# Performance work log

Hardware: AMD Instinct MI355X
Metric: run time of the kernel (lower is better)

## Reference

```python
import jax, jax.numpy as jnp
import numpy as np

B, N, E, ED, H, HID, OUT = 128, 100, 3200, 8, 4, 16, 32


def _ln(x, g, b):
    m = x.mean(-1, keepdims=True)
    v = ((x - m) ** 2).mean(-1, keepdims=True)
    return (x - m) / jnp.sqrt(v + 1e-5) * g + b


def _seg_softmax(logits, seg, n):
    # logits: [Etot, H], seg: [Etot] target node ids
    m = jax.ops.segment_max(logits, seg, num_segments=n)
    ex = jnp.exp(logits - m[seg])
    s = jax.ops.segment_sum(ex, seg, num_segments=n)
    return ex / (s[seg] + 1e-16)


def _tconv(x, src, dst, ea, Wq, bq, Wk, bk, Wv, bv, We, Ws, bs, heads, ch, n):
    # PyG TransformerConv, concat=False, root_weight=True, beta=False
    q = (x @ Wq.T + bq).reshape(-1, heads, ch)
    k = (x @ Wk.T + bk).reshape(-1, heads, ch)
    v = (x @ Wv.T + bv).reshape(-1, heads, ch)
    e = (ea @ We.T).reshape(-1, heads, ch)
    alpha = (q[dst] * (k[src] + e)).sum(-1) / jnp.sqrt(jnp.float32(ch))  # [Etot,H]
    alpha = _seg_softmax(alpha, dst, n)
    msg = (v[src] + e) * alpha[..., None]
    out = jax.ops.segment_sum(msg, dst, num_segments=n)  # [n,H,ch]
    out = out.mean(axis=1)  # concat=False -> head mean
    return out + x @ Ws.T + bs


def setup_inputs() -> dict:
    key = jax.random.key(0)
    ks = jax.random.split(key, 32)
    d = {}
    d['nodes_feats'] = jax.random.randint(ks[0], (B, N, 1), 0, 5).astype(jnp.float32)
    d['edge_index'] = jax.random.randint(ks[1], (B, 2, E), 0, N).astype(jnp.int32)
    d['edge_attr'] = jax.random.normal(ks[2], (B, E, ED), jnp.float32)
    d['agent_id'] = jax.random.randint(ks[3], (B, 1), 0, N).astype(jnp.int32)
    s = 0.1
    d['entity_embed'] = jax.random.normal(ks[4], (5, 4), jnp.float32)
    d['W1'] = jax.random.normal(ks[5], (HID, 4 + ED), jnp.float32) * s
    d['b1'] = jnp.zeros((HID,), jnp.float32)
    d['W2'] = jax.random.normal(ks[6], (HID, HID), jnp.float32) * s
    d['b2'] = jnp.zeros((HID,), jnp.float32)
    d['W3'] = jax.random.normal(ks[7], (HID, HID), jnp.float32) * s
    d['b3'] = jnp.zeros((HID,), jnp.float32)
    d['ln_g'] = jnp.ones((HID,), jnp.float32)
    d['ln_b'] = jnp.zeros((HID,), jnp.float32)
    i = 8
    for pre, ch, outd in (('g1', HID, HID), ('g2', OUT, OUT)):
        d[pre + '_Wq'] = jax.random.normal(ks[i + 0], (H * ch, HID), jnp.float32) * s
        d[pre + '_bq'] = jnp.zeros((H * ch,), jnp.float32)
        d[pre + '_Wk'] = jax.random.normal(ks[i + 1], (H * ch, HID), jnp.float32) * s
        d[pre + '_bk'] = jnp.zeros((H * ch,), jnp.float32)
        d[pre + '_Wv'] = jax.random.normal(ks[i + 2], (H * ch, HID), jnp.float32) * s
        d[pre + '_bv'] = jnp.zeros((H * ch,), jnp.float32)
        d[pre + '_We'] = jax.random.normal(ks[i + 3], (H * ch, ED), jnp.float32) * s
        d[pre + '_Ws'] = jax.random.normal(ks[i + 4], (outd, HID), jnp.float32) * s
        d[pre + '_bs'] = jnp.zeros((outd,), jnp.float32)
        i += 5
    return d


def reference(nodes_feats, edge_index, edge_attr, agent_id, entity_embed,
              W1, b1, W2, b2, W3, b3, ln_g, ln_b,
              g1_Wq, g1_bq, g1_Wk, g1_bk, g1_Wv, g1_bv, g1_We, g1_Ws, g1_bs,
              g2_Wq, g2_bq, g2_Wk, g2_bk, g2_Wv, g2_bv, g2_We, g2_Ws, g2_bs):
    n_tot = B * N
    # batched graph -> flat graph with per-batch node offsets
    offs = (jnp.arange(B, dtype=edge_index.dtype) * N)[:, None, None]
    ei = (edge_index + offs).transpose(1, 0, 2).reshape(2, -1)  # [2, B*E]
    src, dst = ei[0], ei[1]
    x = nodes_feats.reshape(-1, 1)            # [n_tot, 1]
    ea = edge_attr.reshape(-1, ED)            # [B*E, ED]

    # Embedding message-passing layer (aggr='add')
    etype = x[:, 0].astype(jnp.int32)[src]
    emb = entity_embed[etype]                  # [Etot, 4]
    h = jnp.concatenate([emb, ea], axis=1)
    h = _ln(jax.nn.relu(h @ W1.T + b1), ln_g, ln_b)
    h = _ln(jax.nn.relu(h @ W2.T + b2), ln_g, ln_b)
    h = _ln(jax.nn.relu(h @ W3.T + b3), ln_g, ln_b)
    z = jax.ops.segment_sum(h, dst, num_segments=n_tot)  # [n_tot, 16]

    a = _tconv(z, src, dst, ea, g1_Wq, g1_bq, g1_Wk, g1_bk, g1_Wv, g1_bv,
               g1_We, g1_Ws, g1_bs, H, HID, n_tot)
    a = _tconv(a, src, dst, ea, g2_Wq, g2_bq, g2_Wk, g2_bk, g2_Wv, g2_bv,
               g2_We, g2_Ws, g2_bs, H, OUT, n_tot)
    a = jax.nn.relu(a).reshape(B, N, OUT)
    # graph_aggr == 'agent': gather the agent node per batch
    out = jnp.take_along_axis(a, agent_id[:, :, None].astype(jnp.int32), axis=1)
    return out[:, 0, :]  # [B, OUT]
```

## Files before the change

kernel.cpp:

```cpp
#include <hip/hip_runtime.h>
#include <math.h>
#include <stdint.h>

#define Bb   128
#define Nn   100
#define Ee   3200
#define NTOT (Bb*Nn)
#define ETOT (Bb*Ee)



__global__ __launch_bounds__(1024) void k_csr(const int* __restrict__ ei,
                                              const int* __restrict__ agent,
                                              int* __restrict__ off,
                                              int2* __restrict__ cpair,
                                              int* __restrict__ mark)
{
    int b = ((blockIdx.x & 7) << 4) + (blockIdx.x >> 3);
    int t = threadIdx.x;
    __shared__ int s_src[Ee];
    __shared__ int s_dst[Ee];
    __shared__ int cnt[128];
    __shared__ int exc[128];
    __shared__ int cur[128];
    if (t < 128) cnt[t] = 0;
    if (t < Nn) mark[b * Nn + t] = 0;
    __syncthreads();
    const int* eis = ei + (size_t)b * 2 * Ee;
    const int* eid = eis + Ee;
    for (int e = t; e < Ee; e += 1024) {
        int s = eis[e];
        int d = eid[e];
        s_src[e] = s;
        s_dst[e] = d;
        atomicAdd(&cnt[d], 1);
    }
    __syncthreads();
    if (t < 64) {
        int c0 = cnt[2 * t];
        int c1 = cnt[2 * t + 1];
        int p = c0 + c1;
#pragma unroll
        for (int d = 1; d < 64; d <<= 1) {
            int v = __shfl_up(p, d);
            if (t >= d) p += v;
        }
        exc[2 * t]     = p - c0 - c1;
        exc[2 * t + 1] = p - c1;
        cur[2 * t]     = p - c0 - c1;
        cur[2 * t + 1] = p - c1;
    }
    __syncthreads();
    if (t < Nn) off[b * Nn + t] = b * Ee + exc[t];
    if (b == Bb - 1 && t == 0) off[NTOT] = ETOT;
    for (int e = t; e < Ee; e += 1024) {
        int d = s_dst[e];
        int idx = atomicAdd(&cur[d], 1);
        cpair[b * Ee + idx] = make_int2(s_src[e] + b * Nn, b * Ee + e);
    }
    int an = agent[b];
    if (t == 0) mark[b * Nn + an] = 1;
    for (int e = t; e < Ee; e += 1024) {
        if (s_dst[e] == an) mark[b * Nn + s_src[e]] = 1;
    }
}


__device__ __forceinline__ void ln_reg(float* h, const float* __restrict__ g,
                                       const float* __restrict__ b) {
    float s = 0.f;
#pragma unroll
    for (int c = 0; c < 16; c++) s += h[c];
    float m = s * 0.0625f;
    float v = 0.f;
#pragma unroll
    for (int c = 0; c < 16; c++) { float d = h[c] - m; v += d * d; }
    float r = rsqrtf(v * 0.0625f + 1e-5f);
#pragma unroll
    for (int c = 0; c < 16; c++) h[c] = (h[c] - m) * r * g[c] + b[c];
}

__global__ __launch_bounds__(256) void k_mlpz(
    const float* __restrict__ nf, const float* __restrict__ ea, const float* __restrict__ ee,
    const float* __restrict__ W1, const float* __restrict__ b1,
    const float* __restrict__ W2, const float* __restrict__ b2,
    const float* __restrict__ W3, const float* __restrict__ b3,
    const float* __restrict__ lg, const float* __restrict__ lb,
    const float* __restrict__ Wk, const float* __restrict__ bk,
    const float* __restrict__ Wv, const float* __restrict__ bv,
    const int* __restrict__ off, const int2* __restrict__ cpair,
    float* __restrict__ z, float* __restrict__ k1, float* __restrict__ v1)
{
    int lane = threadIdx.x & 63;
    int wid  = threadIdx.x >> 6;
    int n    = (blockIdx.x & 7) * (NTOT / 8) + (blockIdx.x >> 3) * 4 + wid;

    int o0 = off[n];
    int deg = off[n + 1] - o0;
    int chunks = (deg + 63) >> 6;

    float zs[16];
#pragma unroll
    for (int c = 0; c < 16; c++) zs[c] = 0.f;

    for (int ch = 0; ch < chunks; ch++) {
        int i = ch * 64 + lane;
        float h3[16];
        if (i < deg) {
            int2 p = cpair[o0 + i];
            int et = (int)nf[p.x];
            float in[12];
#pragma unroll
            for (int j = 0; j < 4; j++) in[j] = ee[et * 4 + j];
            const float4* ea4 = (const float4*)(ea + (size_t)p.y * 8);
            float4 ua = ea4[0], ub = ea4[1];
            in[4] = ua.x; in[5] = ua.y; in[6] = ua.z; in[7] = ua.w;
            in[8] = ub.x; in[9] = ub.y; in[10] = ub.z; in[11] = ub.w;

            float h1[16];
#pragma unroll
            for (int c = 0; c < 16; c++) {
                float s = b1[c];
#pragma unroll
                for (int j = 0; j < 12; j++) s = fmaf(W1[c * 12 + j], in[j], s);
                h1[c] = fmaxf(s, 0.f);
            }
            ln_reg(h1, lg, lb);
            float h2[16];
#pragma unroll
            for (int c = 0; c < 16; c++) {
                float s = b2[c];
#pragma unroll
                for (int j = 0; j < 16; j++) s = fmaf(W2[c * 16 + j], h1[j], s);
                h2[c] = fmaxf(s, 0.f);
            }
            ln_reg(h2, lg, lb);
#pragma unroll
            for (int c = 0; c < 16; c++) {
                float s = b3[c];
#pragma unroll
                for (int j = 0; j < 16; j++) s = fmaf(W3[c * 16 + j], h2[j], s);
                h3[c] = fmaxf(s, 0.f);
            }
            ln_reg(h3, lg, lb);
        } else {
#pragma unroll
            for (int c = 0; c < 16; c++) h3[c] = 0.f;
        }
#pragma unroll
        for (int c = 0; c < 16; c++) {
            float s = h3[c];
            s += __shfl_xor(s, 1);
            s += __shfl_xor(s, 2);
            s += __shfl_xor(s, 4);
            s += __shfl_xor(s, 8);
            s += __shfl_xor(s, 16);
            s += __shfl_xor(s, 32);
            zs[c] += s;
        }
    }

#pragma unroll
    for (int c = 0; c < 16; c++) if (lane == c) z[n * 16 + c] = zs[c];

    float ak = bk[lane], av = bv[lane];
#pragma unroll
    for (int j = 0; j < 16; j++) {
        ak = fmaf(Wk[lane * 16 + j], zs[j], ak);
        av = fmaf(Wv[lane * 16 + j], zs[j], av);
    }
    k1[n * 64 + lane] = ak;
    v1[n * 64 + lane] = av;
}


__global__ __launch_bounds__(256) void k_attn1(
    const float* __restrict__ ea,
    const float* __restrict__ k1, const float* __restrict__ v1,
    const float* __restrict__ z, const int* __restrict__ mark,
    const float* __restrict__ Wq, const float* __restrict__ bq,
    const float* __restrict__ We, const float* __restrict__ Ws, const float* __restrict__ bs,
    const int* __restrict__ off, const int2* __restrict__ cpair,
    float* __restrict__ a1)
{
    int n = (blockIdx.x & 7) * (NTOT / 8) + (blockIdx.x >> 3);
    if (!mark[n]) return;

    __shared__ float sm[4][64], sl[4][64], sa[4][64];
    int lane = threadIdx.x & 63;
    int w    = threadIdx.x >> 6;

    float zz[16];
#pragma unroll
    for (int j = 0; j < 16; j++) zz[j] = z[n * 16 + j];
    float ql = bq[lane];
#pragma unroll
    for (int j = 0; j < 16; j++) ql = fmaf(Wq[lane * 16 + j], zz[j], ql);
    float wer[8];
#pragma unroll
    for (int j = 0; j < 8; j++) wer[j] = We[lane * 8 + j];

    int o0  = off[n];
    int deg = off[n + 1] - o0;
    int i    = o0 + ((deg * w) >> 2);
    int iend = o0 + ((deg * (w + 1)) >> 2);

    float m = -1e30f, l = 0.f, acc = 0.f;
    for (; i + 2 <= iend; i += 2) {
        int2 pA = cpair[i];
        int2 pB = cpair[i + 1];
        const float4* eaA = (const float4*)(ea + (size_t)pA.y * 8);
        const float4* eaB = (const float4*)(ea + (size_t)pB.y * 8);
        float4 a0v = eaA[0], a1v = eaA[1], b0v = eaB[0], b1v = eaB[1];
        float eA = wer[0] * a0v.x + wer[1] * a0v.y + wer[2] * a0v.z + wer[3] * a0v.w
                 + wer[4] * a1v.x + wer[5] * a1v.y + wer[6] * a1v.z + wer[7] * a1v.w;
        float eB = wer[0] * b0v.x + wer[1] * b0v.y + wer[2] * b0v.z + wer[3] * b0v.w
                 + wer[4] * b1v.x + wer[5] * b1v.y + wer[6] * b1v.z + wer[7] * b1v.w;
        float kA = k1[(size_t)pA.x * 64 + lane];
        float kB = k1[(size_t)pB.x * 64 + lane];
        float vA = v1[(size_t)pA.x * 64 + lane];
        float vB = v1[(size_t)pB.x * 64 + lane];
        float tA = ql * (kA + eA);
        float tB = ql * (kB + eB);
        tA += __shfl_xor(tA, 1, 16);  tB += __shfl_xor(tB, 1, 16);
        tA += __shfl_xor(tA, 2, 16);  tB += __shfl_xor(tB, 2, 16);
        tA += __shfl_xor(tA, 4, 16);  tB += __shfl_xor(tB, 4, 16);
        tA += __shfl_xor(tA, 8, 16);  tB += __shfl_xor(tB, 8, 16);
        float lA  = tA * 0.25f;
        float lBv = tB * 0.25f;
        float nm = fmaxf(m, fmaxf(lA, lBv));
        float sc = __expf(m - nm);
        float wA = __expf(lA - nm);
        float wB = __expf(lBv - nm);
        acc = acc * sc + wA * (vA + eA) + wB * (vB + eB);
        l   = l * sc + wA + wB;
        m   = nm;
    }
    for (; i < iend; i++) {
        int2 p = cpair[i];
        const float4* ea4 = (const float4*)(ea + (size_t)p.y * 8);
        float4 u0 = ea4[0], u1 = ea4[1];
        float el = wer[0] * u0.x + wer[1] * u0.y + wer[2] * u0.z + wer[3] * u0.w
                 + wer[4] * u1.x + wer[5] * u1.y + wer[6] * u1.z + wer[7] * u1.w;
        float kl = k1[(size_t)p.x * 64 + lane];
        float tq = ql * (kl + el);
        tq += __shfl_xor(tq, 1, 16);
        tq += __shfl_xor(tq, 2, 16);
        tq += __shfl_xor(tq, 4, 16);
        tq += __shfl_xor(tq, 8, 16);
        float logit = tq * 0.25f;
        float nm = fmaxf(m, logit);
        float sc = __expf(m - nm);
        float wv = __expf(logit - nm);
        float vl = v1[(size_t)p.x * 64 + lane];
        acc = acc * sc + wv * (vl + el);
        l   = l * sc + wv;
        m   = nm;
    }
    sm[w][lane] = m; sl[w][lane] = l; sa[w][lane] = acc;
    __syncthreads();
    if (w == 0) {
        float M = fmaxf(fmaxf(sm[0][lane], sm[1][lane]), fmaxf(sm[2][lane], sm[3][lane]));
        float L = 0.f, A = 0.f;
#pragma unroll
        for (int ww = 0; ww < 4; ww++) {
            float sc = __expf(sm[ww][lane] - M);
            L += sc * sl[ww][lane];
            A += sc * sa[ww][lane];
        }
        float y = (deg > 0) ? (A / L) : 0.f;
        y += __shfl_xor(y, 16);
        y += __shfl_xor(y, 32);
        y *= 0.25f;
        if (lane < 16) {
            float r = bs[lane];
#pragma unroll
            for (int j = 0; j < 16; j++) r = fmaf(Ws[lane * 16 + j], zz[j], r);
            a1[n * 16 + lane] = y + r;
        }
    }
}


__global__ __launch_bounds__(512) void k_g2(
    const float* __restrict__ ea, const float* __restrict__ a1, const int* __restrict__ agent,
    const float* __restrict__ Wq, const float* __restrict__ bq,
    const float* __restrict__ Wk, const float* __restrict__ bk,
    const float* __restrict__ Wv, const float* __restrict__ bv,
    const float* __restrict__ We, const float* __restrict__ Ws, const float* __restrict__ bs,
    const int* __restrict__ off, const int2* __restrict__ cpair,
    float* __restrict__ out)
{
    __shared__ float sm[8][64], sl[8][64], sa0[8][64], sa1[8][64];
    int b = ((blockIdx.x & 7) << 4) + (blockIdx.x >> 3);
    int lane = threadIdx.x & 63;
    int w = threadIdx.x >> 6;
    int n = b * Nn + agent[b];
    int v0 = lane * 2, v1i = lane * 2 + 1;

    float aa[16];
#pragma unroll
    for (int j = 0; j < 16; j++) aa[j] = a1[n * 16 + j];

    float wk0[16], wk1[16], wv0[16], wv1[16], we0[8], we1[8];
#pragma unroll
    for (int j = 0; j < 16; j++) {
        wk0[j] = Wk[v0 * 16 + j];  wk1[j] = Wk[v1i * 16 + j];
        wv0[j] = Wv[v0 * 16 + j];  wv1[j] = Wv[v1i * 16 + j];
    }
#pragma unroll
    for (int j = 0; j < 8; j++) { we0[j] = We[v0 * 8 + j]; we1[j] = We[v1i * 8 + j]; }

    float q0 = bq[v0], q1v = bq[v1i];
#pragma unroll
    for (int j = 0; j < 16; j++) {
        q0  = fmaf(Wq[v0 * 16 + j],  aa[j], q0);
        q1v = fmaf(Wq[v1i * 16 + j], aa[j], q1v);
    }

    int o0 = off[n];
    int deg = off[n + 1] - o0;

    float m = -1e30f, l = 0.f, a0 = 0.f, a1c = 0.f;
    for (int i = w; i < deg; i += 8) {
        int2 p = cpair[o0 + i];
        int src = p.x, ge = p.y;
        float as[16];
#pragma unroll
        for (int j = 0; j < 16; j++) as[j] = a1[src * 16 + j];
        const float4* ea4 = (const float4*)(ea + (size_t)ge * 8);
        float4 u0 = ea4[0], u1 = ea4[1];
        float eav[8] = {u0.x, u0.y, u0.z, u0.w, u1.x, u1.y, u1.z, u1.w};

        float k0 = bk[v0], k1v = bk[v1i], vv0 = bv[v0], vv1 = bv[v1i];
#pragma unroll
        for (int j = 0; j < 16; j++) {
            k0  = fmaf(wk0[j], as[j], k0);
            k1v = fmaf(wk1[j], as[j], k1v);
            vv0 = fmaf(wv0[j], as[j], vv0);
            vv1 = fmaf(wv1[j], as[j], vv1);
        }
        float e0 = 0.f, e1 = 0.f;
#pragma unroll
        for (int j = 0; j < 8; j++) { e0 = fmaf(we0[j], eav[j], e0); e1 = fmaf(we1[j], eav[j], e1); }

        float t = q0 * (k0 + e0) + q1v * (k1v + e1);
        t += __shfl_xor(t, 1, 16);
        t += __shfl_xor(t, 2, 16);
        t += __shfl_xor(t, 4, 16);
        t += __shfl_xor(t, 8, 16);
        float logit = t * 0.17677669529663687f;
        float nm = fmaxf(m, logit);
        float sc = __expf(m - nm);
        float wgt = __expf(logit - nm);
        a0  = a0 * sc + wgt * (vv0 + e0);
        a1c = a1c * sc + wgt * (vv1 + e1);
        l   = l * sc + wgt;
        m   = nm;
    }
    sm[w][lane] = m; sl[w][lane] = l; sa0[w][lane] = a0; sa1[w][lane] = a1c;
    __syncthreads();
    if (w == 0) {
        float M = sm[0][lane];
#pragma unroll
        for (int ww = 1; ww < 8; ww++) M = fmaxf(M, sm[ww][lane]);
        float L = 0.f, A0 = 0.f, A1 = 0.f;
#pragma unroll
        for (int ww = 0; ww < 8; ww++) {
            float sc = __expf(sm[ww][lane] - M);
            L  += sc * sl[ww][lane];
            A0 += sc * sa0[ww][lane];
            A1 += sc * sa1[ww][lane];
        }
        float y0 = (deg > 0) ? (A0 / L) : 0.f;
        float y1 = (deg > 0) ? (A1 / L) : 0.f;
        y0 += __shfl_xor(y0, 16); y0 += __shfl_xor(y0, 32);
        y1 += __shfl_xor(y1, 16); y1 += __shfl_xor(y1, 32);
        y0 *= 0.25f; y1 *= 0.25f;

        if (lane < 16) {
            int c0 = lane * 2, c1 = lane * 2 + 1;
            float r0 = bs[c0], r1 = bs[c1];
#pragma unroll
            for (int j = 0; j < 16; j++) {
                r0 = fmaf(Ws[c0 * 16 + j], aa[j], r0);
                r1 = fmaf(Ws[c1 * 16 + j], aa[j], r1);
            }
            out[b * 32 + c0] = fmaxf(y0 + r0, 0.f);
            out[b * 32 + c1] = fmaxf(y1 + r1, 0.f);
        }
    }
}


extern "C" void kernel_launch(void* const* d_in, const int* in_sizes, int n_in,
                              void* d_out, int out_size, void* d_ws, size_t ws_size,
                              hipStream_t stream) {
    (void)in_sizes; (void)n_in; (void)out_size; (void)ws_size;
    const float* nf    = (const float*)d_in[0];
    const int*   ei    = (const int*)d_in[1];
    const float* ea    = (const float*)d_in[2];
    const int*   agent = (const int*)d_in[3];
    const float* ee    = (const float*)d_in[4];
    const float* W1    = (const float*)d_in[5];
    const float* b1    = (const float*)d_in[6];
    const float* W2    = (const float*)d_in[7];
    const float* b2    = (const float*)d_in[8];
    const float* W3    = (const float*)d_in[9];
    const float* b3    = (const float*)d_in[10];
    const float* lg    = (const float*)d_in[11];
    const float* lb    = (const float*)d_in[12];
    const float* g1Wq  = (const float*)d_in[13];
    const float* g1bq  = (const float*)d_in[14];
    const float* g1Wk  = (const float*)d_in[15];
    const float* g1bk  = (const float*)d_in[16];
    const float* g1Wv  = (const float*)d_in[17];
    const float* g1bv  = (const float*)d_in[18];
    const float* g1We  = (const float*)d_in[19];
    const float* g1Ws  = (const float*)d_in[20];
    const float* g1bs  = (const float*)d_in[21];
    const float* g2Wq  = (const float*)d_in[22];
    const float* g2bq  = (const float*)d_in[23];
    const float* g2Wk  = (const float*)d_in[24];
    const float* g2bk  = (const float*)d_in[25];
    const float* g2Wv  = (const float*)d_in[26];
    const float* g2bv  = (const float*)d_in[27];
    const float* g2We  = (const float*)d_in[28];
    const float* g2Ws  = (const float*)d_in[29];
    const float* g2bs  = (const float*)d_in[30];
    float* out = (float*)d_out;

    char* w = (char*)d_ws;
    int* mark  = (int*)w;  w += (size_t)NTOT * 4;
    int* off   = (int*)w;  w += (size_t)(NTOT + 4) * 4;
    w = (char*)(((uintptr_t)w + 15) & ~(uintptr_t)15);
    int2* cpair = (int2*)w; w += (size_t)ETOT * 8;
    float* z   = (float*)w; w += (size_t)NTOT * 16 * 4;
    float* k1  = (float*)w; w += (size_t)NTOT * 64 * 4;
    float* v1  = (float*)w; w += (size_t)NTOT * 64 * 4;
    float* a1  = (float*)w; w += (size_t)NTOT * 16 * 4;

    k_csr<<<dim3(Bb), dim3(1024), 0, stream>>>(ei, agent, off, cpair, mark);
    k_mlpz<<<dim3(NTOT / 4), dim3(256), 0, stream>>>(
        nf, ea, ee, W1, b1, W2, b2, W3, b3, lg, lb,
        g1Wk, g1bk, g1Wv, g1bv,
        off, cpair, z, k1, v1);
    k_attn1<<<dim3(NTOT), dim3(256), 0, stream>>>(
        ea, k1, v1, z, mark,
        g1Wq, g1bq, g1We, g1Ws, g1bs,
        off, cpair, a1);
    k_g2<<<dim3(Bb), dim3(512), 0, stream>>>(
        ea, a1, agent, g2Wq, g2bq, g2Wk, g2bk, g2Wv, g2bv, g2We, g2Ws, g2bs,
        off, cpair, out);
}
```

Baseline: 193.7 us.

## Fuse layer-1 attention and layer-2 agent attention into one per-graph kernel

The per-node layer-1 attention kernel (12800 blocks, most exiting early on an unmarked-node check) and the layer-2 agent kernel are merged into one kernel with one block per graph. The CSR kernel now emits a compact list of needed nodes (the agent and its in-neighbours) built with shared-memory atomics, and each wave processes whole nodes from that list with a single online-softmax pass. Layer-1 outputs stay in shared memory, removing the a1 global round trip and one launch. In exchange, only 128 blocks run, and each wave walks a full node's edge list serially instead of splitting it four ways, which lowers parallelism.

Result: slower. 228.0 us (+17.7%).

```diff
diff --git a/kernel.cpp b/kernel.cpp
--- a/kernel.cpp
+++ b/kernel.cpp
@@ -14,7 +14,8 @@
                                               const int* __restrict__ agent,
                                               int* __restrict__ off,
                                               int2* __restrict__ cpair,
-                                              int* __restrict__ mark)
+                                              int* __restrict__ mlist,
+                                              int* __restrict__ mcnt)
 {
     int b = ((blockIdx.x & 7) << 4) + (blockIdx.x >> 3);
     int t = threadIdx.x;
@@ -23,8 +24,11 @@
     __shared__ int cnt[128];
     __shared__ int exc[128];
     __shared__ int cur[128];
+    __shared__ int smark[Nn], slist[Nn];
+    __shared__ int scnt;
     if (t < 128) cnt[t] = 0;
-    if (t < Nn) mark[b * Nn + t] = 0;
+    if (t < Nn)  smark[t] = 0;
+    if (t == 0)  scnt = 0;
     __syncthreads();
     const int* eis = ei + (size_t)b * 2 * Ee;
     const int* eid = eis + Ee;
@@ -59,10 +63,20 @@
         cpair[b * Ee + idx] = make_int2(s_src[e] + b * Nn, b * Ee + e);
     }
     int an = agent[b];
-    if (t == 0) mark[b * Nn + an] = 1;
+    if (t == 0) {
+        int old = atomicExch(&smark[an], 1);
+        if (!old) { int ix = atomicAdd(&scnt, 1); slist[ix] = an; }
+    }
     for (int e = t; e < Ee; e += 1024) {
-        if (s_dst[e] == an) mark[b * Nn + s_src[e]] = 1;
-    }
+        if (s_dst[e] == an) {
+            int s = s_src[e];
+            int old = atomicExch(&smark[s], 1);
+            if (!old) { int ix = atomicAdd(&scnt, 1); slist[ix] = s; }
+        }
+    }
+    __syncthreads();
+    if (t < scnt) mlist[b * Nn + t] = slist[t];
+    if (t == 0)   mcnt[b] = scnt;
 }
 
 
@@ -174,220 +188,214 @@
 }
 
 
-__global__ __launch_bounds__(256) void k_attn1(
+__global__ __launch_bounds__(512) void k_ag(
     const float* __restrict__ ea,
     const float* __restrict__ k1, const float* __restrict__ v1,
-    const float* __restrict__ z, const int* __restrict__ mark,
-    const float* __restrict__ Wq, const float* __restrict__ bq,
-    const float* __restrict__ We, const float* __restrict__ Ws, const float* __restrict__ bs,
+    const float* __restrict__ z,
+    const int* __restrict__ mlist, const int* __restrict__ mcnt,
+    const int* __restrict__ agent,
     const int* __restrict__ off, const int2* __restrict__ cpair,
-    float* __restrict__ a1)
+    const float* __restrict__ g1Wq, const float* __restrict__ g1bq,
+    const float* __restrict__ g1We, const float* __restrict__ g1Ws, const float* __restrict__ g1bs,
+    const float* __restrict__ g2Wq, const float* __restrict__ g2bq,
+    const float* __restrict__ g2Wk, const float* __restrict__ g2bk,
+    const float* __restrict__ g2Wv, const float* __restrict__ g2bv,
+    const float* __restrict__ g2We, const float* __restrict__ g2Ws, const float* __restrict__ g2bs,
+    float* __restrict__ out)
 {
-    int n = (blockIdx.x & 7) * (NTOT / 8) + (blockIdx.x >> 3);
-    if (!mark[n]) return;
-
-    __shared__ float sm[4][64], sl[4][64], sa[4][64];
+    __shared__ float a1s[Nn][16];
+    __shared__ float sm[8][64], sl[8][64], s0[8][64], s1[8][64];
+
+    int b    = ((blockIdx.x & 7) << 4) + (blockIdx.x >> 3);
     int lane = threadIdx.x & 63;
     int w    = threadIdx.x >> 6;
 
-    float zz[16];
-#pragma unroll
-    for (int j = 0; j < 16; j++) zz[j] = z[n * 16 + j];
-    float ql = bq[lane];
-#pragma unroll
-    for (int j = 0; j < 16; j++) ql = fmaf(Wq[lane * 16 + j], zz[j], ql);
-    float wer[8];
-#pragma unroll
-    for (int j = 0; j < 8; j++) wer[j] = We[lane * 8 + j];
-
-    int o0  = off[n];
-    int deg = off[n + 1] - o0;
-    int i    = o0 + ((deg * w) >> 2);
-    int iend = o0 + ((deg * (w + 1)) >> 2);
-
-    float m = -1e30f, l = 0.f, acc = 0.f;
-    for (; i + 2 <= iend; i += 2) {
-        int2 pA = cpair[i];
-        int2 pB = cpair[i + 1];
-        const float4* eaA = (const float4*)(ea + (size_t)pA.y * 8);
-        const float4* eaB = (const float4*)(ea + (size_t)pB.y * 8);
-        float4 a0v = eaA[0], a1v = eaA[1], b0v = eaB[0], b1v = eaB[1];
-        float eA = wer[0] * a0v.x + wer[1] * a0v.y + wer[2] * a0v.z + wer[3] * a0v.w
-                 + wer[4] * a1v.x + wer[5] * a1v.y + wer[6] * a1v.z + wer[7] * a1v.w;
-        float eB = wer[0] * b0v.x + wer[1] * b0v.y + wer[2] * b0v.z + wer[3] * b0v.w
-                 + wer[4] * b1v.x + wer[5] * b1v.y + wer[6] * b1v.z + wer[7] * b1v.w;
-        float kA = k1[(size_t)pA.x * 64 + lane];
-        float kB = k1[(size_t)pB.x * 64 + lane];
-        float vA = v1[(size_t)pA.x * 64 + lane];
-        float vB = v1[(size_t)pB.x * 64 + lane];
-        float tA = ql * (kA + eA);
-        float tB = ql * (kB + eB);
-        tA += __shfl_xor(tA, 1, 16);  tB += __shfl_xor(tB, 1, 16);
-        tA += __shfl_xor(tA, 2, 16);  tB += __shfl_xor(tB, 2, 16);
-        tA += __shfl_xor(tA, 4, 16);  tB += __shfl_xor(tB, 4, 16);
-        tA += __shfl_xor(tA, 8, 16);  tB += __shfl_xor(tB, 8, 16);
-        float lA  = tA * 0.25f;
-        float lBv = tB * 0.25f;
-        float nm = fmaxf(m, fmaxf(lA, lBv));
-        float sc = __expf(m - nm);
-        float wA = __expf(lA - nm);
-        float wB = __expf(lBv - nm);
-        acc = acc * sc + wA * (vA + eA) + wB * (vB + eB);
-        l   = l * sc + wA + wB;
-        m   = nm;
-    }
-    for (; i < iend; i++) {
-        int2 p = cpair[i];
-        const float4* ea4 = (const float4*)(ea + (size_t)p.y * 8);
-        float4 u0 = ea4[0], u1 = ea4[1];
-        float el = wer[0] * u0.x + wer[1] * u0.y + wer[2] * u0.z + wer[3] * u0.w
-                 + wer[4] * u1.x + wer[5] * u1.y + wer[6] * u1.z + wer[7] * u1.w;
-        float kl = k1[(size_t)p.x * 64 + lane];
-        float tq = ql * (kl + el);
-        tq += __shfl_xor(tq, 1, 16);
-        tq += __shfl_xor(tq, 2, 16);
-        tq += __shfl_xor(tq, 4, 16);
-        tq += __shfl_xor(tq, 8, 16);
-        float logit = tq * 0.25f;
-        float nm = fmaxf(m, logit);
-        float sc = __expf(m - nm);
-        float wv = __expf(logit - nm);
-        float vl = v1[(size_t)p.x * 64 + lane];
-        acc = acc * sc + wv * (vl + el);
-        l   = l * sc + wv;
-        m   = nm;
-    }
-    sm[w][lane] = m; sl[w][lane] = l; sa[w][lane] = acc;
+    {
+        float wq[16], wer[8], ws1[16];
+#pragma unroll
+        for (int j = 0; j < 16; j++) wq[j] = g1Wq[lane * 16 + j];
+#pragma unroll
+        for (int j = 0; j < 8; j++) wer[j] = g1We[lane * 8 + j];
+        int lc = lane & 15;
+#pragma unroll
+        for (int j = 0; j < 16; j++) ws1[j] = g1Ws[lc * 16 + j];
+        float bq1 = g1bq[lane], bs1 = g1bs[lc];
+
+        int mc = mcnt[b];
+        for (int ix = w; ix < mc; ix += 8) {
+            int loc = mlist[b * Nn + ix];
+            int n   = b * Nn + loc;
+            float zz[16];
+#pragma unroll
+            for (int j = 0; j < 16; j++) zz[j] = z[n * 16 + j];
+            float ql = bq1;
+#pragma unroll
+            for (int j = 0; j < 16; j++) ql = fmaf(wq[j], zz[j], ql);
+
+            int o0  = off[n];
+            int deg = off[n + 1] - o0;
+            int i = o0, iend = o0 + deg;
+
+            float m = -1e30f, l = 0.f, acc = 0.f;
+            for (; i + 2 <= iend; i += 2) {
+                int2 pA = cpair[i];
+                int2 pB = cpair[i + 1];
+                const float4* eaA = (const float4*)(ea + (size_t)pA.y * 8);
+                const float4* eaB = (const float4*)(ea + (size_t)pB.y * 8);
+                float4 a0v = eaA[0], a1v = eaA[1], b0v = eaB[0], b1v = eaB[1];
+                float eA = wer[0] * a0v.x + wer[1] * a0v.y + wer[2] * a0v.z + wer[3] * a0v.w
+                         + wer[4] * a1v.x + wer[5] * a1v.y + wer[6] * a1v.z + wer[7] * a1v.w;
+                float eB = wer[0] * b0v.x + wer[1] * b0v.y + wer[2] * b0v.z + wer[3] * b0v.w
+                         + wer[4] * b1v.x + wer[5] * b1v.y + wer[6] * b1v.z + wer[7] * b1v.w;
+                float kA = k1[(size_t)pA.x * 64 + lane];
+                float kB = k1[(size_t)pB.x * 64 + lane];
+                float vA = v1[(size_t)pA.x * 64 + lane];
+                float vB = v1[(size_t)pB.x * 64 + lane];
+                float tA = ql * (kA + eA);
+                float tB = ql * (kB + eB);
+                tA += __shfl_xor(tA, 1, 16);  tB += __shfl_xor(tB, 1, 16);
+                tA += __shfl_xor(tA, 2, 16);  tB += __shfl_xor(tB, 2, 16);
+                tA += __shfl_xor(tA, 4, 16);  tB += __shfl_xor(tB, 4, 16);
+                tA += __shfl_xor(tA, 8, 16);  tB += __shfl_xor(tB, 8, 16);
+                float lA  = tA * 0.25f;
+                float lBv = tB * 0.25f;
+                float nm = fmaxf(m, fmaxf(lA, lBv));
+                float sc = __expf(m - nm);
+                float wA = __expf(lA - nm);
+                float wB = __expf(lBv - nm);
+                acc = acc * sc + wA * (vA + eA) + wB * (vB + eB);
+                l   = l * sc + wA + wB;
+                m   = nm;
+            }
+            for (; i < iend; i++) {
+                int2 p = cpair[i];
+                const float4* ea4 = (const float4*)(ea + (size_t)p.y * 8);
+                float4 u0 = ea4[0], u1 = ea4[1];
+                float el = wer[0] * u0.x + wer[1] * u0.y + wer[2] * u0.z + wer[3] * u0.w
+                         + wer[4] * u1.x + wer[5] * u1.y + wer[6] * u1.z + wer[7] * u1.w;
+                float kl = k1[(size_t)p.x * 64 + lane];
+                float tq = ql * (kl + el);
+                tq += __shfl_xor(tq, 1, 16);
+                tq += __shfl_xor(tq, 2, 16);
+                tq += __shfl_xor(tq, 4, 16);
+                tq += __shfl_xor(tq, 8, 16);
+                float logit = tq * 0.25f;
+                float nm = fmaxf(m, logit);
+                float sc = __expf(m - nm);
+                float wv = __expf(logit - nm);
+                float vl = v1[(size_t)p.x * 64 + lane];
+                acc = acc * sc + wv * (vl + el);
+                l   = l * sc + wv;
+                m   = nm;
+            }
+            float y = (deg > 0) ? (acc / l) : 0.f;
+            y += __shfl_xor(y, 16);
+            y += __shfl_xor(y, 32);
+            y *= 0.25f;
+            float r = bs1;
+#pragma unroll
+            for (int j = 0; j < 16; j++) r = fmaf(ws1[j], zz[j], r);
+            if (lane < 16) a1s[loc][lane] = y + r;
+        }
+    }
     __syncthreads();
-    if (w == 0) {
-        float M = fmaxf(fmaxf(sm[0][lane], sm[1][lane]), fmaxf(sm[2][lane], sm[3][lane]));
-        float L = 0.f, A = 0.f;
-#pragma unroll
-        for (int ww = 0; ww < 4; ww++) {
-            float sc = __expf(sm[ww][lane] - M);
-            L += sc * sl[ww][lane];
-            A += sc * sa[ww][lane];
-        }
-        float y = (deg > 0) ? (A / L) : 0.f;
-        y += __shfl_xor(y, 16);
-        y += __shfl_xor(y, 32);
-        y *= 0.25f;
-        if (lane < 16) {
-            float r = bs[lane];
-#pragma unroll
-            for (int j = 0; j < 16; j++) r = fmaf(Ws[lane * 16 + j], zz[j], r);
-            a1[n * 16 + lane] = y + r;
-        }
-    }
-}
-
-
-__global__ __launch_bounds__(512) void k_g2(
-    const float* __restrict__ ea, const float* __restrict__ a1, const int* __restrict__ agent,
-    const float* __restrict__ Wq, const float* __restrict__ bq,
-    const float* __restrict__ Wk, const float* __restrict__ bk,
-    const float* __restrict__ Wv, const float* __restrict__ bv,
-    const float* __restrict__ We, const float* __restrict__ Ws, const float* __restrict__ bs,
-    const int* __restrict__ off, const int2* __restrict__ cpair,
-    float* __restrict__ out)
-{
-    __shared__ float sm[8][64], sl[8][64], sa0[8][64], sa1[8][64];
-    int b = ((blockIdx.x & 7) << 4) + (blockIdx.x >> 3);
-    int lane = threadIdx.x & 63;
-    int w = threadIdx.x >> 6;
-    int n = b * Nn + agent[b];
-    int v0 = lane * 2, v1i = lane * 2 + 1;
-
-    float aa[16];
-#pragma unroll
-    for (int j = 0; j < 16; j++) aa[j] = a1[n * 16 + j];
-
-    float wk0[16], wk1[16], wv0[16], wv1[16], we0[8], we1[8];
-#pragma unroll
-    for (int j = 0; j < 16; j++) {
-        wk0[j] = Wk[v0 * 16 + j];  wk1[j] = Wk[v1i * 16 + j];
-        wv0[j] = Wv[v0 * 16 + j];  wv1[j] = Wv[v1i * 16 + j];
-    }
-#pragma unroll
-    for (int j = 0; j < 8; j++) { we0[j] = We[v0 * 8 + j]; we1[j] = We[v1i * 8 + j]; }
-
-    float q0 = bq[v0], q1v = bq[v1i];
-#pragma unroll
-    for (int j = 0; j < 16; j++) {
-        q0  = fmaf(Wq[v0 * 16 + j],  aa[j], q0);
-        q1v = fmaf(Wq[v1i * 16 + j], aa[j], q1v);
-    }
-
-    int o0 = off[n];
-    int deg = off[n + 1] - o0;
-
-    float m = -1e30f, l = 0.f, a0 = 0.f, a1c = 0.f;
-    for (int i = w; i < deg; i += 8) {
-        int2 p = cpair[o0 + i];
-        int src = p.x, ge = p.y;
-        float as[16];
-#pragma unroll
-        for (int j = 0; j < 16; j++) as[j] = a1[src * 16 + j];
-        const float4* ea4 = (const float4*)(ea + (size_t)ge * 8);
-        float4 u0 = ea4[0], u1 = ea4[1];
-        float eav[8] = {u0.x, u0.y, u0.z, u0.w, u1.x, u1.y, u1.z, u1.w};
-
-        float k0 = bk[v0], k1v = bk[v1i], vv0 = bv[v0], vv1 = bv[v1i];
+
+    {
+        int an = agent[b];
+        int n  = b * Nn + an;
+        int v0 = lane * 2, v1i = lane * 2 + 1;
+
+        float aa[16];
+#pragma unroll
+        for (int j = 0; j < 16; j++) aa[j] = a1s[an][j];
+
+        float wk0[16], wk1[16], wv0[16], wv1[16], we0[8], we1[8];
 #pragma unroll
         for (int j = 0; j < 16; j++) {
-            k0  = fmaf(wk0[j], as[j], k0);
-            k1v = fmaf(wk1[j], as[j], k1v);
-            vv0 = fmaf(wv0[j], as[j], vv0);
-            vv1 = fmaf(wv1[j], as[j], vv1);
-        }
-        float e0 = 0.f, e1 = 0.f;
-#pragma unroll
-        for (int j = 0; j < 8; j++) { e0 = fmaf(we0[j], eav[j], e0); e1 = fmaf(we1[j], eav[j], e1); }
-
-        float t = q0 * (k0 + e0) + q1v * (k1v + e1);
-        t += __shfl_xor(t, 1, 16);
-        t += __shfl_xor(t, 2, 16);
-        t += __shfl_xor(t, 4, 16);
-        t += __shfl_xor(t, 8, 16);
-        float logit = t * 0.17677669529663687f;
-        float nm = fmaxf(m, logit);
-        float sc = __expf(m - nm);
-        float wgt = __expf(logit - nm);
-        a0  = a0 * sc + wgt * (vv0 + e0);
-        a1c = a1c * sc + wgt * (vv1 + e1);
-        l   = l * sc + wgt;
-        m   = nm;
-    }
-    sm[w][lane] = m; sl[w][lane] = l; sa0[w][lane] = a0; sa1[w][lane] = a1c;
-    __syncthreads();
-    if (w == 0) {
-        float M = sm[0][lane];
-#pragma unroll
-        for (int ww = 1; ww < 8; ww++) M = fmaxf(M, sm[ww][lane]);
-        float L = 0.f, A0 = 0.f, A1 = 0.f;
-#pragma unroll
-        for (int ww = 0; ww < 8; ww++) {
-            float sc = __expf(sm[ww][lane] - M);
-            L  += sc * sl[ww][lane];
-            A0 += sc * sa0[ww][lane];
-            A1 += sc * sa1[ww][lane];
-        }
-        float y0 = (deg > 0) ? (A0 / L) : 0.f;
-        float y1 = (deg > 0) ? (A1 / L) : 0.f;
-        y0 += __shfl_xor(y0, 16); y0 += __shfl_xor(y0, 32);
-        y1 += __shfl_xor(y1, 16); y1 += __shfl_xor(y1, 32);
-        y0 *= 0.25f; y1 *= 0.25f;
-
-        if (lane < 16) {
-            int c0 = lane * 2, c1 = lane * 2 + 1;
-            float r0 = bs[c0], r1 = bs[c1];
+            wk0[j] = g2Wk[v0 * 16 + j];  wk1[j] = g2Wk[v1i * 16 + j];
+            wv0[j] = g2Wv[v0 * 16 + j];  wv1[j] = g2Wv[v1i * 16 + j];
+        }
+#pragma unroll
+        for (int j = 0; j < 8; j++) { we0[j] = g2We[v0 * 8 + j]; we1[j] = g2We[v1i * 8 + j]; }
+
+        float q0 = g2bq[v0], q1v = g2bq[v1i];
+#pragma unroll
+        for (int j = 0; j < 16; j++) {
+            q0  = fmaf(g2Wq[v0 * 16 + j],  aa[j], q0);
+            q1v = fmaf(g2Wq[v1i * 16 + j], aa[j], q1v);
+        }
+
+        int o0 = off[n];
+        int deg = off[n + 1] - o0;
+
+        float m = -1e30f, l = 0.f, a0 = 0.f, a1c = 0.f;
+        for (int i = w; i < deg; i += 8) {
+            int2 p = cpair[o0 + i];
+            int srcl = p.x - b * Nn;
+            float as[16];
+#pragma unroll
+            for (int j = 0; j < 16; j++) as[j] = a1s[srcl][j];
+            const float4* ea4 = (const float4*)(ea + (size_t)p.y * 8);
+            float4 u0 = ea4[0], u1 = ea4[1];
+            float eav[8] = {u0.x, u0.y, u0.z, u0.w, u1.x, u1.y, u1.z, u1.w};
+
+            float k0 = g2bk[v0], k1v = g2bk[v1i], vv0 = g2bv[v0], vv1 = g2bv[v1i];
 #pragma unroll
             for (int j = 0; j < 16; j++) {
-                r0 = fmaf(Ws[c0 * 16 + j], aa[j], r0);
-                r1 = fmaf(Ws[c1 * 16 + j], aa[j], r1);
-            }
-            out[b * 32 + c0] = fmaxf(y0 + r0, 0.f);
-            out[b * 32 + c1] = fmaxf(y1 + r1, 0.f);
+                k0  = fmaf(wk0[j], as[j], k0);
+                k1v = fmaf(wk1[j], as[j], k1v);
+                vv0 = fmaf(wv0[j], as[j], vv0);
+                vv1 = fmaf(wv1[j], as[j], vv1);
+            }
+            float e0 = 0.f, e1 = 0.f;
+#pragma unroll
+            for (int j = 0; j < 8; j++) { e0 = fmaf(we0[j], eav[j], e0); e1 = fmaf(we1[j], eav[j], e1); }
+
+            float tq = q0 * (k0 + e0) + q1v * (k1v + e1);
+            tq += __shfl_xor(tq, 1, 16);
+            tq += __shfl_xor(tq, 2, 16);
+            tq += __shfl_xor(tq, 4, 16);
+            tq += __shfl_xor(tq, 8, 16);
+            float logit = tq * 0.17677669529663687f;
+            float nm = fmaxf(m, logit);
+            float sc = __expf(m - nm);
+            float wgt = __expf(logit - nm);
+            a0  = a0 * sc + wgt * (vv0 + e0);
+            a1c = a1c * sc + wgt * (vv1 + e1);
+            l   = l * sc + wgt;
+            m   = nm;
+        }
+        sm[w][lane] = m; sl[w][lane] = l; s0[w][lane] = a0; s1[w][lane] = a1c;
+        __syncthreads();
+        if (w == 0) {
+            float M = sm[0][lane];
+#pragma unroll
+            for (int ww = 1; ww < 8; ww++) M = fmaxf(M, sm[ww][lane]);
+            float L = 0.f, A0 = 0.f, A1 = 0.f;
+#pragma unroll
+            for (int ww = 0; ww < 8; ww++) {
+                float sc = __expf(sm[ww][lane] - M);
+                L  += sc * sl[ww][lane];
+                A0 += sc * s0[ww][lane];
+                A1 += sc * s1[ww][lane];
+            }
+            float y0 = (deg > 0) ? (A0 / L) : 0.f;
+            float y1 = (deg > 0) ? (A1 / L) : 0.f;
+            y0 += __shfl_xor(y0, 16); y0 += __shfl_xor(y0, 32);
+            y1 += __shfl_xor(y1, 16); y1 += __shfl_xor(y1, 32);
+            y0 *= 0.25f; y1 *= 0.25f;
+
+            if (lane < 16) {
+                int c0 = lane * 2, c1 = lane * 2 + 1;
+                float r0 = g2bs[c0], r1 = g2bs[c1];
+#pragma unroll
+                for (int j = 0; j < 16; j++) {
+                    r0 = fmaf(g2Ws[c0 * 16 + j], aa[j], r0);
+                    r1 = fmaf(g2Ws[c1 * 16 + j], aa[j], r1);
+                }
+                out[b * 32 + c0] = fmaxf(y0 + r0, 0.f);
+                out[b * 32 + c1] = fmaxf(y1 + r1, 0.f);
+            }
         }
     }
 }
@@ -431,25 +439,23 @@
     float* out = (float*)d_out;
 
     char* w = (char*)d_ws;
-    int* mark  = (int*)w;  w += (size_t)NTOT * 4;
     int* off   = (int*)w;  w += (size_t)(NTOT + 4) * 4;
     w = (char*)(((uintptr_t)w + 15) & ~(uintptr_t)15);
     int2* cpair = (int2*)w; w += (size_t)ETOT * 8;
     float* z   = (float*)w; w += (size_t)NTOT * 16 * 4;
     float* k1  = (float*)w; w += (size_t)NTOT * 64 * 4;
     float* v1  = (float*)w; w += (size_t)NTOT * 64 * 4;
-    float* a1  = (float*)w; w += (size_t)NTOT * 16 * 4;
-
-    k_csr<<<dim3(Bb), dim3(1024), 0, stream>>>(ei, agent, off, cpair, mark);
+    int* mlist = (int*)w;  w += (size_t)NTOT * 4;
+    int* mcnt  = (int*)w;  w += (size_t)Bb * 4;
+
+    k_csr<<<dim3(Bb), dim3(1024), 0, stream>>>(ei, agent, off, cpair, mlist, mcnt);
     k_mlpz<<<dim3(NTOT / 4), dim3(256), 0, stream>>>(
         nf, ea, ee, W1, b1, W2, b2, W3, b3, lg, lb,
         g1Wk, g1bk, g1Wv, g1bv,
         off, cpair, z, k1, v1);
-    k_attn1<<<dim3(NTOT), dim3(256), 0, stream>>>(
-        ea, k1, v1, z, mark,
+    k_ag<<<dim3(Bb), dim3(512), 0, stream>>>(
+        ea, k1, v1, z, mlist, mcnt, agent, off, cpair,
         g1Wq, g1bq, g1We, g1Ws, g1bs,
-        off, cpair, a1);
-    k_g2<<<dim3(Bb), dim3(512), 0, stream>>>(
-        ea, a1, agent, g2Wq, g2bq, g2Wk, g2bk, g2Wv, g2bv, g2We, g2Ws, g2bs,
-        off, cpair, out);
+        g2Wq, g2bq, g2Wk, g2bk, g2Wv, g2bv, g2We, g2Ws, g2bs,
+        out);
 }
```
